# Performance work log

Measured on AMD Instinct MI355X. Metric: run time of the kernel, lower is better.

The kernel has to match this reference:

```python
import jax, jax.numpy as jnp
import numpy as np

BOS = 1  # TOKENS['BOS'] assumed


def gru_scan(x_seq, h0, W_ih, W_hh, b_ih, b_hh):
    """PyTorch-style single-layer GRU over time. x_seq: (T,B,H), h0: (B,H)."""
    def step(h, x):
        gi = x @ W_ih.T + b_ih          # (B,3H)
        gh = h @ W_hh.T + b_hh          # (B,3H)
        i_r, i_z, i_n = jnp.split(gi, 3, axis=-1)
        h_r, h_z, h_n = jnp.split(gh, 3, axis=-1)
        r = jax.nn.sigmoid(i_r + h_r)
        z = jax.nn.sigmoid(i_z + h_z)
        n = jnp.tanh(i_n + r * h_n)
        h_new = (1.0 - z) * n + z * h
        return h_new, h_new
    hT, outs = jax.lax.scan(step, h0, x_seq)
    return outs, hT


def setup_inputs() -> dict:
    key = jax.random.key(0)
    ks = jax.random.split(key, 24)
    H = 256
    V = 50003       # user_size + 3
    TAGV = 966
    T_in, T_tgt, T_tag, B = 50, 40, 20, 32
    s = 0.02
    inp = {
        'input_tensor': jax.random.randint(ks[0], (T_in, B), 0, V),
        'target_tensor': jax.random.randint(ks[1], (T_tgt, B), 0, V),
        'tag_tensor': jax.random.randint(ks[2], (T_tag, B), 0, TAGV),
        'enc_emb': jax.random.normal(ks[3], (V, H), jnp.float32) * s,
        'enc_Wih': jax.random.normal(ks[4], (3 * H, H), jnp.float32) * s,
        'enc_Whh': jax.random.normal(ks[5], (3 * H, H), jnp.float32) * s,
        'enc_bih': jax.random.normal(ks[6], (3 * H,), jnp.float32) * s,
        'enc_bhh': jax.random.normal(ks[7], (3 * H,), jnp.float32) * s,
        'tag_emb': jax.random.normal(ks[8], (TAGV, H), jnp.float32) * s,
        'tag_Wih': jax.random.normal(ks[9], (3 * H, H), jnp.float32) * s,
        'tag_Whh': jax.random.normal(ks[10], (3 * H, H), jnp.float32) * s,
        'tag_bih': jax.random.normal(ks[11], (3 * H,), jnp.float32) * s,
        'tag_bhh': jax.random.normal(ks[12], (3 * H,), jnp.float32) * s,
        'proj_W': jax.random.normal(ks[13], (H, 2 * H), jnp.float32) * s,
        'proj_b': jax.random.normal(ks[14], (H,), jnp.float32) * s,
        'dec_Wih': jax.random.normal(ks[15], (3 * H, H), jnp.float32) * s,
        'dec_Whh': jax.random.normal(ks[16], (3 * H, H), jnp.float32) * s,
        'dec_bih': jax.random.normal(ks[17], (3 * H,), jnp.float32) * s,
        'dec_bhh': jax.random.normal(ks[18], (3 * H,), jnp.float32) * s,
        'out_W': jax.random.normal(ks[19], (V, H), jnp.float32) * s,
        'out_b': jax.random.normal(ks[20], (V,), jnp.float32) * s,
    }
    return inp


def reference(input_tensor, target_tensor, tag_tensor,
              enc_emb, enc_Wih, enc_Whh, enc_bih, enc_bhh,
              tag_emb, tag_Wih, tag_Whh, tag_bih, tag_bhh,
              proj_W, proj_b,
              dec_Wih, dec_Whh, dec_bih, dec_bhh,
              out_W, out_b):
    T_in, B = input_tensor.shape
    T_tgt = target_tensor.shape[0]
    H = enc_emb.shape[1]
    h0 = jnp.zeros((B, H), enc_emb.dtype)

    # encoder over input tokens
    _, enc_h = gru_scan(enc_emb[input_tensor], h0, enc_Wih, enc_Whh, enc_bih, enc_bhh)
    # tag encoder
    _, tag_h = gru_scan(tag_emb[tag_tensor], h0, tag_Wih, tag_Whh, tag_bih, tag_bhh)

    # proj(cat(tag_hidden, encoder_hidden)); dropout = identity (eval)
    merged = jnp.concatenate([tag_h, enc_h], axis=-1) @ proj_W.T + proj_b  # (B,H)

    # teacher forcing: decoder inputs = [BOS, target[:-1]]
    dec_in = jnp.concatenate(
        [jnp.full((1, B), BOS, dtype=target_tensor.dtype), target_tensor[:-1]], axis=0)
    dec_x = jax.nn.relu(enc_emb[dec_in])                 # (T_tgt,B,H), shared embedding
    dec_outs, _ = gru_scan(dec_x, merged, dec_Wih, dec_Whh, dec_bih, dec_bhh)
    logits = dec_outs @ out_W.T + out_b                  # (T_tgt,B,V)

    # criterion = CrossEntropyLoss(mean over batch), summed over timesteps
    logp = jax.nn.log_softmax(logits, axis=-1)
    nll = -jnp.take_along_axis(logp, target_tensor[..., None], axis=-1)[..., 0]  # (T_tgt,B)
    decoder_loss = nll.mean(axis=1).sum()
    avg_loss = decoder_loss / T_tgt
    decoder_outputs = logits[:, None, :, :]              # (T_tgt,1,B,V) like torch.stack of unsqueezed
    return (decoder_loss, avg_loss, decoder_outputs)
```

## Files before the change

kernel.cpp:

```cpp
#include <hip/hip_runtime.h>
#include <hip/hip_bf16.h>
#include <math.h>


#define H 256
#define H3 768
#define NBATCH 32
#define TIN 50
#define TTGT 40
#define TTAG 20
#define VSZ 50003
#define VP 50048
#define NT 782
#define MT 1280
#define NGIET 210
#define NCVT2 504

typedef float f32x4 __attribute__((ext_vector_type(4)));
typedef short short8 __attribute__((ext_vector_type(8)));

__device__ __forceinline__ float dot4(float4 a, float4 b) {
    return a.x * b.x + a.y * b.y + a.z * b.z + a.w * b.w;
}

__device__ __forceinline__ float bf2f(short s) {
    unsigned int u = ((unsigned int)(unsigned short)s) << 16;
    return __builtin_bit_cast(float, u);
}

__device__ __forceinline__ void bar_lgkm() {
    asm volatile("s_waitcnt lgkmcnt(0)" ::: "memory");
    __builtin_amdgcn_s_barrier();
    __builtin_amdgcn_sched_barrier(0);
}

__global__ void k_prep(const float* eWih, const float* tWih, const float* dWih,
                       float* d0, float* d1, float* d2) {
    int which = blockIdx.y;
    const float* s = which == 0 ? eWih : (which == 1 ? tWih : dWih);
    float* d = which == 0 ? d0 : (which == 1 ? d1 : d2);
    int n = blockIdx.x;
    for (int k = threadIdx.x; k < H; k += 256)
        d[(size_t)(k >> 2) * (H3 * 4) + n * 4 + (k & 3)] = s[(size_t)n * H + k];
}

__global__ __launch_bounds__(256) void k_gi_prep(
    const int* in_toks, const int* tag_toks, const float* enc_emb,
    const float* tag_emb, const float* W4e, const float* W4t,
    const float* bih_e, const float* bhh_e, const float* bih_t,
    const float* bhh_t, __hip_bfloat16* gi_e, __hip_bfloat16* gi_t,
    const float* eWhh, const float* tWhh, const float* dWhh,
    __hip_bfloat16* p0, __hip_bfloat16* p1, __hip_bfloat16* p2,
    const float* projW, float* W4_proj) {
    int bx = blockIdx.x, tid = threadIdx.x;
    if (bx >= 498) {
        int n = bx - 498;
        for (int k = tid; k < 2 * H; k += 256)
            W4_proj[(size_t)(k >> 2) * 1024 + n * 4 + (k & 3)] =
                projW[(size_t)n * 2 * H + k];
        return;
    }
    if (bx >= NGIET) {
        int wb = bx - NGIET;
        int m = wb / 96;
        const float* s = m == 0 ? eWhh : (m == 1 ? tWhh : dWhh);
        __hip_bfloat16* d = m == 0 ? p0 : (m == 1 ? p1 : p2);
        int idx = (wb % 96) * 256 + tid;
        int lane = idx & 63;
        int f = (idx >> 6) % 24;
        int w = idx / (24 * 64);
        int ks = f / 3, q = f % 3;
        int row = (q << 8) + (w << 4) + (lane & 15);
        int k = (ks << 5) + ((lane >> 4) << 3);
#pragma unroll
        for (int j = 0; j < 8; ++j)
            d[(size_t)idx * 8 + j] = __float2bfloat16(s[(size_t)row * H + k + j]);
        return;
    }
    __shared__ float x[NBATCH][H];
    int g = bx % 3, tt = bx / 3;
    const int* toks;
    const float* emb;
    const float* W4;
    const float* bihp;
    const float* bhhp;
    __hip_bfloat16* gip;
    int t;
    if (tt < TIN) {
        toks = in_toks; emb = enc_emb; W4 = W4e; bihp = bih_e; bhhp = bhh_e;
        gip = gi_e; t = tt;
    } else {
        toks = tag_toks; emb = tag_emb; W4 = W4t; bihp = bih_t; bhhp = bhh_t;
        gip = gi_t; t = tt - TIN;
    }
    for (int b = 0; b < NBATCH; ++b)
        x[b][tid] = emb[(size_t)toks[t * NBATCH + b] * H + tid];
    __syncthreads();
    int nb_ = tid & 63, mg = tid >> 6;
    float acc[4][8];
#pragma unroll
    for (int j = 0; j < 4; ++j)
#pragma unroll
        for (int mi = 0; mi < 8; ++mi) acc[j][mi] = 0.f;
    for (int k4 = 0; k4 < 64; ++k4) {
        const float4* wrow = (const float4*)(W4 + (size_t)k4 * 3072);
        float4 w0 = wrow[g * 256 + nb_];
        float4 w1 = wrow[g * 256 + nb_ + 64];
        float4 w2 = wrow[g * 256 + nb_ + 128];
        float4 w3 = wrow[g * 256 + nb_ + 192];
#pragma unroll
        for (int mi = 0; mi < 8; ++mi) {
            float4 xv = *(const float4*)&x[mg * 8 + mi][k4 * 4];
            acc[0][mi] += dot4(xv, w0);
            acc[1][mi] += dot4(xv, w1);
            acc[2][mi] += dot4(xv, w2);
            acc[3][mi] += dot4(xv, w3);
        }
    }
#pragma unroll
    for (int j = 0; j < 4; ++j) {
        int n = g * 256 + nb_ + j * 64;
        float bv = bihp[n] + (g < 2 ? bhhp[n] : 0.0f);
        int nn = n & 255;
        int ww = nn >> 4, lrr = nn & 15;
#pragma unroll
        for (int mi = 0; mi < 8; ++mi) {
            int bm = mg * 8 + mi;
            int locb = bm >> 4, lmm = bm & 15;
            int lgg = lmm >> 2, reg = lmm & 3;
            size_t idx = ((size_t)(t * 2 + locb) * 16 + ww) * 1024 +
                         reg * 256 + (lgg * 16 + lrr) * 4 + g;
            gip[idx] = __float2bfloat16(acc[j][mi] + bv);
        }
    }
}

__global__ __launch_bounds__(1024) void k_scan_enc(
    const __hip_bfloat16* gi1, const __hip_bfloat16* W1, const float* bhh1,
    float* hT1, int T1,
    const __hip_bfloat16* gi2, const __hip_bfloat16* W2, const float* bhh2,
    float* hT2, int T2,
    const int* tgt_toks, const float* enc_emb, const float* W4d,
    const float* bih_d, const float* bhh_d, __hip_bfloat16* gi_d,
    const float* outW, __hip_bfloat16* outWb) {
    __shared__ uint4 WL[16 * 6 * 64];
    __shared__ uint4 HBF[2][512];

    int blk = blockIdx.x, tid = threadIdx.x;
    if (blk >= 4) {
        int wb = blk - 4;
        if (wb < TTGT) {
            int t = wb;
            float* x = (float*)WL;
            if (tid < 256) {
                for (int b = 0; b < NBATCH; ++b) {
                    int tok = (t == 0) ? 1 : tgt_toks[(t - 1) * NBATCH + b];
                    x[b * 256 + tid] = fmaxf(enc_emb[(size_t)tok * H + tid], 0.0f);
                }
            }
            __syncthreads();
            if (tid < 768) {
                int g = tid >> 8, tidg = tid & 255;
                int nb_ = tidg & 63, mg = tidg >> 6;
                float acc[4][8];
#pragma unroll
                for (int j = 0; j < 4; ++j)
#pragma unroll
                    for (int mi = 0; mi < 8; ++mi) acc[j][mi] = 0.f;
                for (int k4 = 0; k4 < 64; ++k4) {
                    const float4* wrow = (const float4*)(W4d + (size_t)k4 * 3072);
                    float4 w0 = wrow[g * 256 + nb_];
                    float4 w1 = wrow[g * 256 + nb_ + 64];
                    float4 w2 = wrow[g * 256 + nb_ + 128];
                    float4 w3 = wrow[g * 256 + nb_ + 192];
#pragma unroll
                    for (int mi = 0; mi < 8; ++mi) {
                        float4 xv = *(const float4*)&x[(mg * 8 + mi) * 256 + k4 * 4];
                        acc[0][mi] += dot4(xv, w0);
                        acc[1][mi] += dot4(xv, w1);
                        acc[2][mi] += dot4(xv, w2);
                        acc[3][mi] += dot4(xv, w3);
                    }
                }
#pragma unroll
                for (int j = 0; j < 4; ++j) {
                    int n = g * 256 + nb_ + j * 64;
                    float bv = bih_d[n] + (g < 2 ? bhh_d[n] : 0.0f);
                    int nn = n & 255;
                    int ww = nn >> 4, lrr = nn & 15;
#pragma unroll
                    for (int mi = 0; mi < 8; ++mi) {
                        int bm = mg * 8 + mi;
                        int locb = bm >> 4, lmm = bm & 15;
                        int lgg = lmm >> 2, reg = lmm & 3;
                        size_t idx = ((size_t)(t * 2 + locb) * 16 + ww) * 1024 +
                                     reg * 256 + (lgg * 16 + lrr) * 4 + g;
                        gi_d[idx] = __float2bfloat16(acc[j][mi] + bv);
                    }
                }
            }
            return;
        }
        const size_t total = (size_t)VP * H / 4;
        const size_t stride = (size_t)NCVT2 * 1024;
        for (size_t i = (size_t)(wb - TTGT) * 1024 + tid; i < total; i += stride) {
            size_t i4 = i * 4;
            int row = (int)(i4 >> 8);
            float4 v;
            if (row < VSZ) v = *(const float4*)(outW + i4);
            else v = make_float4(0.f, 0.f, 0.f, 0.f);
            outWb[i4 + 0] = __float2bfloat16(v.x);
            outWb[i4 + 1] = __float2bfloat16(v.y);
            outWb[i4 + 2] = __float2bfloat16(v.z);
            outWb[i4 + 3] = __float2bfloat16(v.w);
        }
        return;
    }

    const __hip_bfloat16 *gip, *Wg;
    const float* bhh;
    float* hTp;
    int T, loc;
    if (blk < 2) {
        gip = gi1; Wg = W1; bhh = bhh1; hTp = hT1; T = T1; loc = blk;
    } else {
        gip = gi2; Wg = W2; bhh = bhh2; hTp = hT2; T = T2; loc = blk - 2;
    }
    int mb = loc * 16;
    int w = tid >> 6, lane = tid & 63, lr = lane & 15, lg = lane >> 4;

    short8 wreg[18];
    const uint4* Wg4 = (const uint4*)Wg;
#pragma unroll
    for (int f = 0; f < 18; ++f) {
        uint4 v = Wg4[(size_t)(w * 24 + f) * 64 + lane];
        wreg[f] = *(short8*)&v;
    }
#pragma unroll
    for (int i = 0; i < 6; ++i)
        WL[(w * 6 + i) * 64 + lane] = Wg4[(size_t)(w * 24 + 18 + i) * 64 + lane];

    float bnv = bhh[512 + w * 16 + lr];

    float hprev[4];
    short* HB16 = (short*)HBF;
#pragma unroll
    for (int reg = 0; reg < 4; ++reg) {
        int row = lg * 4 + reg;
        hprev[reg] = 0.0f;
        int ch = w * 2 + (lr >> 3);
        int slot = ch ^ (row & 7);
        HB16[row * 256 + slot * 8 + (lr & 7)] = 0;
    }
    uint2 gv[4];
    {
        const __hip_bfloat16* gp = gip + ((size_t)loc * 16 + w) * 1024;
#pragma unroll
        for (int reg = 0; reg < 4; ++reg)
            gv[reg] = *(const uint2*)(gp + reg * 256 + lane * 4);
    }
    __syncthreads();

    const short8* HSbase = (const short8*)HBF;
    const short8* WLs = (const short8*)WL;
    for (int t = 0; t < T; ++t) {
        int p = t & 1, p2 = p ^ 1;
        const short8* HS = HSbase + p * 512;
        f32x4 acc[3];
        acc[0] = (f32x4){0.f, 0.f, 0.f, 0.f};
        acc[1] = acc[0];
        acc[2] = (f32x4){bnv, bnv, bnv, bnv};
#pragma unroll
        for (int ks = 0; ks < 6; ++ks) {
            short8 a = HS[lr * 32 + ((ks * 4 + lg) ^ (lr & 7))];
#pragma unroll
            for (int q = 0; q < 3; ++q)
                acc[q] = __builtin_amdgcn_mfma_f32_16x16x32_bf16(
                    a, wreg[ks * 3 + q], acc[q], 0, 0, 0);
        }
#pragma unroll
        for (int ks = 6; ks < 8; ++ks) {
            short8 a = HS[lr * 32 + ((ks * 4 + lg) ^ (lr & 7))];
#pragma unroll
            for (int q = 0; q < 3; ++q) {
                short8 bv = WLs[(w * 6 + (ks - 6) * 3 + q) * 64 + lane];
                acc[q] = __builtin_amdgcn_mfma_f32_16x16x32_bf16(
                    a, bv, acc[q], 0, 0, 0);
            }
        }
#pragma unroll
        for (int reg = 0; reg < 4; ++reg) {
            uint2 u = gv[reg];
            float gr = bf2f((short)(u.x & 0xffff));
            float gz = bf2f((short)(u.x >> 16));
            float gn = bf2f((short)(u.y & 0xffff));
            float er = __expf(-(gr + acc[0][reg]));
            float r = __builtin_amdgcn_rcpf(1.0f + er);
            float ez = __expf(-(gz + acc[1][reg]));
            float z = __builtin_amdgcn_rcpf(1.0f + ez);
            float xx = gn + r * acc[2][reg];
            float e2 = __expf(-2.0f * fabsf(xx));
            float nv = copysignf((1.0f - e2) * __builtin_amdgcn_rcpf(1.0f + e2), xx);
            float hnew = (1.0f - z) * nv + z * hprev[reg];
            hprev[reg] = hnew;
            __hip_bfloat16 qb = __float2bfloat16(hnew);
            int row = lg * 4 + reg;
            int ch = w * 2 + (lr >> 3);
            int slot = ch ^ (row & 7);
            HB16[p2 * 4096 + row * 256 + slot * 8 + (lr & 7)] = *(short*)&qb;
        }
        if (t + 1 < T) {
            const __hip_bfloat16* gp =
                gip + ((size_t)((t + 1) * 2 + loc) * 16 + w) * 1024;
#pragma unroll
            for (int reg = 0; reg < 4; ++reg)
                gv[reg] = *(const uint2*)(gp + reg * 256 + lane * 4);
        }
        bar_lgkm();
    }
    if (hTp) {
#pragma unroll
        for (int reg = 0; reg < 4; ++reg) {
            int row = lg * 4 + reg, col = w * 16 + lr;
            hTp[(size_t)(mb + row) * H + col] = hprev[reg];
        }
    }
}

__global__ __launch_bounds__(1024) void k_scan_dec(
    const __hip_bfloat16* gip, const __hip_bfloat16* Wg, const float* bhh,
    __hip_bfloat16* outp, int T,
    const float* tagh, const float* ench, const float* W4p, const float* pb) {
    __shared__ uint4 WL[16 * 6 * 64];
    __shared__ uint4 HBF[2][512];

    int blk = blockIdx.x, tid = threadIdx.x;
    int loc = blk, mb = loc * 16;
    int w = tid >> 6, lane = tid & 63, lr = lane & 15, lg = lane >> 4;

    float* CC = (float*)WL;
    float* MM = ((float*)WL) + 8192;
#pragma unroll
    for (int i = 0; i < 8; ++i) {
        int idx = i * 1024 + tid;
        int row = idx >> 9, col = idx & 511;
        float v = (col < 256) ? tagh[(size_t)(mb + row) * H + col]
                              : ench[(size_t)(mb + row) * H + (col - 256)];
        CC[idx] = v;
    }
    __syncthreads();
    {
        int col = tid & 255, rg = tid >> 8;
        float a0 = 0.f, a1 = 0.f, a2 = 0.f, a3 = 0.f;
        for (int k4 = 0; k4 < 128; ++k4) {
            float4 wv = ((const float4*)(W4p + (size_t)k4 * 1024))[col];
            float4 c0 = *(const float4*)&CC[(rg * 4 + 0) * 512 + k4 * 4];
            float4 c1 = *(const float4*)&CC[(rg * 4 + 1) * 512 + k4 * 4];
            float4 c2 = *(const float4*)&CC[(rg * 4 + 2) * 512 + k4 * 4];
            float4 c3 = *(const float4*)&CC[(rg * 4 + 3) * 512 + k4 * 4];
            a0 += dot4(c0, wv);
            a1 += dot4(c1, wv);
            a2 += dot4(c2, wv);
            a3 += dot4(c3, wv);
        }
        float bv = pb[col];
        __syncthreads();
        MM[(rg * 4 + 0) * 256 + col] = a0 + bv;
        MM[(rg * 4 + 1) * 256 + col] = a1 + bv;
        MM[(rg * 4 + 2) * 256 + col] = a2 + bv;
        MM[(rg * 4 + 3) * 256 + col] = a3 + bv;
    }
    __syncthreads();

    float hprev[4];
    short* HB16 = (short*)HBF;
#pragma unroll
    for (int reg = 0; reg < 4; ++reg) {
        int row = lg * 4 + reg, col = w * 16 + lr;
        float hv = MM[row * 256 + col];
        hprev[reg] = hv;
        __hip_bfloat16 q = __float2bfloat16(hv);
        int ch = w * 2 + (lr >> 3);
        int slot = ch ^ (row & 7);
        HB16[row * 256 + slot * 8 + (lr & 7)] = *(short*)&q;
    }
    __syncthreads();

    short8 wreg[18];
    const uint4* Wg4 = (const uint4*)Wg;
#pragma unroll
    for (int f = 0; f < 18; ++f) {
        uint4 v = Wg4[(size_t)(w * 24 + f) * 64 + lane];
        wreg[f] = *(short8*)&v;
    }
#pragma unroll
    for (int i = 0; i < 6; ++i)
        WL[(w * 6 + i) * 64 + lane] = Wg4[(size_t)(w * 24 + 18 + i) * 64 + lane];

    float bnv = bhh[512 + w * 16 + lr];

    uint2 gv[4];
    {
        const __hip_bfloat16* gp = gip + ((size_t)loc * 16 + w) * 1024;
#pragma unroll
        for (int reg = 0; reg < 4; ++reg)
            gv[reg] = *(const uint2*)(gp + reg * 256 + lane * 4);
    }
    __syncthreads();

    const short8* HSbase = (const short8*)HBF;
    const short8* WLs = (const short8*)WL;
    for (int t = 0; t < T; ++t) {
        int p = t & 1, p2 = p ^ 1;
        const short8* HS = HSbase + p * 512;
        f32x4 acc[3];
        acc[0] = (f32x4){0.f, 0.f, 0.f, 0.f};
        acc[1] = acc[0];
        acc[2] = (f32x4){bnv, bnv, bnv, bnv};
#pragma unroll
        for (int ks = 0; ks < 6; ++ks) {
            short8 a = HS[lr * 32 + ((ks * 4 + lg) ^ (lr & 7))];
#pragma unroll
            for (int q = 0; q < 3; ++q)
                acc[q] = __builtin_amdgcn_mfma_f32_16x16x32_bf16(
                    a, wreg[ks * 3 + q], acc[q], 0, 0, 0);
        }
#pragma unroll
        for (int ks = 6; ks < 8; ++ks) {
            short8 a = HS[lr * 32 + ((ks * 4 + lg) ^ (lr & 7))];
#pragma unroll
            for (int q = 0; q < 3; ++q) {
                short8 bv = WLs[(w * 6 + (ks - 6) * 3 + q) * 64 + lane];
                acc[q] = __builtin_amdgcn_mfma_f32_16x16x32_bf16(
                    a, bv, acc[q], 0, 0, 0);
            }
        }
#pragma unroll
        for (int reg = 0; reg < 4; ++reg) {
            uint2 u = gv[reg];
            float gr = bf2f((short)(u.x & 0xffff));
            float gz = bf2f((short)(u.x >> 16));
            float gn = bf2f((short)(u.y & 0xffff));
            float er = __expf(-(gr + acc[0][reg]));
            float r = __builtin_amdgcn_rcpf(1.0f + er);
            float ez = __expf(-(gz + acc[1][reg]));
            float z = __builtin_amdgcn_rcpf(1.0f + ez);
            float xx = gn + r * acc[2][reg];
            float e2 = __expf(-2.0f * fabsf(xx));
            float nv = copysignf((1.0f - e2) * __builtin_amdgcn_rcpf(1.0f + e2), xx);
            float hnew = (1.0f - z) * nv + z * hprev[reg];
            hprev[reg] = hnew;
            __hip_bfloat16 qb = __float2bfloat16(hnew);
            int row = lg * 4 + reg;
            int ch = w * 2 + (lr >> 3);
            int slot = ch ^ (row & 7);
            HB16[p2 * 4096 + row * 256 + slot * 8 + (lr & 7)] = *(short*)&qb;
        }
        if (t + 1 < T) {
            const __hip_bfloat16* gp =
                gip + ((size_t)((t + 1) * 2 + loc) * 16 + w) * 1024;
#pragma unroll
            for (int reg = 0; reg < 4; ++reg)
                gv[reg] = *(const uint2*)(gp + reg * 256 + lane * 4);
        }
        if (t >= 1 && tid < 512) {
            int lb = tid >> 5, ch2 = tid & 31;
            short8 hv = HSbase[p * 512 + lb * 32 + (ch2 ^ (lb & 7))];
            *(short8*)(outp + (size_t)((t - 1) * NBATCH + mb + lb) * H + ch2 * 8) = hv;
        }
        bar_lgkm();
    }
    if (tid < 512) {
        int lb = tid >> 5, ch2 = tid & 31;
        short8 hv = HSbase[(T & 1) * 512 + lb * 32 + (ch2 ^ (lb & 7))];
        *(short8*)(outp + (size_t)((T - 1) * NBATCH + mb + lb) * H + ch2 * 8) = hv;
    }
}

__global__ __launch_bounds__(256) void k_logits(const __hip_bfloat16* A,
                                                const __hip_bfloat16* Bw,
                                                const float* bias, float* dout,
                                                float* pmax, float* psum) {
    __shared__ uint4 bsm[2048];
    __shared__ float cst[4][16][68];
    int bid = blockIdx.x;
    int wg = (bid & 7) * 1955 + (bid >> 3);
    int nblk = wg / 20, mblk = wg % 20;
    int m0 = mblk * 64, n0 = nblk * 64;
    int tid = threadIdx.x;
    int wave = tid >> 6, lane = tid & 63, lr = lane & 15, lg = lane >> 4;
    const uint4* Bg = (const uint4*)(Bw + (size_t)n0 * H);
#pragma unroll
    for (int i = 0; i < 8; ++i) {
        int c = tid + i * 256;
        int r = c >> 5, g = c & 31;
        bsm[(r << 5) | (g ^ (r & 7))] = Bg[c];
    }
    short8 areg[8];
    const uint4* Ar = (const uint4*)(A + (size_t)(m0 + wave * 16 + lr) * H);
#pragma unroll
    for (int ks = 0; ks < 8; ++ks) {
        uint4 v = Ar[ks * 4 + lg];
        areg[ks] = *(short8*)&v;
    }
    float biasv[4];
    bool valid[4];
#pragma unroll
    for (int ns = 0; ns < 4; ++ns) {
        int n = n0 + ns * 16 + lr;
        valid[ns] = (n < VSZ);
        biasv[ns] = valid[ns] ? bias[n] : 0.f;
    }
    __syncthreads();
    f32x4 acc[4];
#pragma unroll
    for (int ns = 0; ns < 4; ++ns) acc[ns] = (f32x4){0.f, 0.f, 0.f, 0.f};
    const short8* L = (const short8*)bsm;
#pragma unroll
    for (int ks = 0; ks < 8; ++ks) {
        int ga = ks * 4 + lg;
#pragma unroll
        for (int ns = 0; ns < 4; ++ns) {
            int rb = ns * 16 + lr;
            acc[ns] = __builtin_amdgcn_mfma_f32_16x16x32_bf16(
                areg[ks], L[(rb << 5) | (ga ^ (rb & 7))], acc[ns], 0, 0, 0);
        }
    }
    float* cw = &cst[wave][0][0];
#pragma unroll
    for (int reg = 0; reg < 4; ++reg) {
        int m = m0 + wave * 16 + lg * 4 + reg;
        float v[4];
        float rm = -INFINITY;
#pragma unroll
        for (int ns = 0; ns < 4; ++ns) {
            v[ns] = acc[ns][reg] + biasv[ns];
            if (valid[ns]) rm = fmaxf(rm, v[ns]);
            cw[(lg * 4 + reg) * 68 + ns * 16 + lr] = v[ns];
        }
        for (int off = 1; off < 16; off <<= 1) rm = fmaxf(rm, __shfl_xor(rm, off));
        float se = 0.f;
#pragma unroll
        for (int ns = 0; ns < 4; ++ns)
            if (valid[ns]) se += __expf(v[ns] - rm);
        for (int off = 1; off < 16; off <<= 1) se += __shfl_xor(se, off);
        if (lr == 0) {
            pmax[(size_t)m * NT + nblk] = rm;
            psum[(size_t)m * NT + nblk] = se;
        }
    }
    float* dbase = dout + 2 + (size_t)(m0 + wave * 16) * VSZ + n0;
    int c0 = lr * 4;
    bool full = (n0 + c0 + 3 < VSZ);
#pragma unroll
    for (int it = 0; it < 4; ++it) {
        int row = it * 4 + lg;
        f32x4 v4 = *(const f32x4*)&cst[wave][row][c0];
        float* p = dbase + (size_t)row * VSZ + c0;
        if (full) {
            __builtin_memcpy(p, &v4, 16);
        } else {
#pragma unroll
            for (int j = 0; j < 4; ++j)
                if (n0 + c0 + j < VSZ) p[j] = v4[j];
        }
    }
}

__global__ void k_lse(const float* pmax, const float* psum, float* lse) {
    int m = blockIdx.x, tid = threadIdx.x;
    __shared__ float sm[4];
    float lm = -INFINITY;
    for (int i = tid; i < NT; i += 256) lm = fmaxf(lm, pmax[(size_t)m * NT + i]);
    for (int off = 1; off < 64; off <<= 1) lm = fmaxf(lm, __shfl_xor(lm, off));
    if ((tid & 63) == 0) sm[tid >> 6] = lm;
    __syncthreads();
    float M = fmaxf(fmaxf(sm[0], sm[1]), fmaxf(sm[2], sm[3]));
    __syncthreads();
    float s = 0.f;
    for (int i = tid; i < NT; i += 256)
        s += psum[(size_t)m * NT + i] * __expf(pmax[(size_t)m * NT + i] - M);
    for (int off = 1; off < 64; off <<= 1) s += __shfl_xor(s, off);
    if ((tid & 63) == 0) sm[tid >> 6] = s;
    __syncthreads();
    if (tid == 0) lse[m] = M + logf(sm[0] + sm[1] + sm[2] + sm[3]);
}

__global__ void k_loss(const float* lse, const int* tgt, float* dout) {
    int tid = threadIdx.x;
    __shared__ float sm[4];
    float s = 0.f;
    for (int m = tid; m < MT; m += 256) {
        int tg = tgt[m];
        s += lse[m] - dout[2 + (size_t)m * VSZ + tg];
    }
    for (int off = 1; off < 64; off <<= 1) s += __shfl_xor(s, off);
    if ((tid & 63) == 0) sm[tid >> 6] = s;
    __syncthreads();
    if (tid == 0) {
        float total = sm[0] + sm[1] + sm[2] + sm[3];
        dout[0] = total / 32.0f;
        dout[1] = total / 1280.0f;
    }
}

extern "C" void kernel_launch(void* const* d_in, const int* in_sizes, int n_in,
                              void* d_out, int out_size, void* d_ws,
                              size_t ws_size, hipStream_t stream) {
    const int* input_tensor = (const int*)d_in[0];
    const int* target_tensor = (const int*)d_in[1];
    const int* tag_tensor = (const int*)d_in[2];
    const float* enc_emb = (const float*)d_in[3];
    const float* enc_Wih = (const float*)d_in[4];
    const float* enc_Whh = (const float*)d_in[5];
    const float* enc_bih = (const float*)d_in[6];
    const float* enc_bhh = (const float*)d_in[7];
    const float* tag_emb = (const float*)d_in[8];
    const float* tag_Wih = (const float*)d_in[9];
    const float* tag_Whh = (const float*)d_in[10];
    const float* tag_bih = (const float*)d_in[11];
    const float* tag_bhh = (const float*)d_in[12];
    const float* proj_W = (const float*)d_in[13];
    const float* proj_b = (const float*)d_in[14];
    const float* dec_Wih = (const float*)d_in[15];
    const float* dec_Whh = (const float*)d_in[16];
    const float* dec_bih = (const float*)d_in[17];
    const float* dec_bhh = (const float*)d_in[18];
    const float* out_W = (const float*)d_in[19];
    const float* out_b = (const float*)d_in[20];

    char* wsb = (char*)d_ws;
    size_t o = 0;
    auto alloc = [&](size_t bytes) {
        size_t r = o;
        o += (bytes + 511) & ~(size_t)511;
        return r;
    };
    float* W4_enc_ih = (float*)(wsb + alloc(H3 * H * 4));
    float* W4_tag_ih = (float*)(wsb + alloc(H3 * H * 4));
    float* W4_dec_ih = (float*)(wsb + alloc(H3 * H * 4));
    float* W4_proj   = (float*)(wsb + alloc(H * 2 * H * 4));
    __hip_bfloat16* gi_enc = (__hip_bfloat16*)(wsb + alloc((size_t)TIN * 65536));
    __hip_bfloat16* gi_tag = (__hip_bfloat16*)(wsb + alloc((size_t)TTAG * 65536));
    __hip_bfloat16* gi_dec = (__hip_bfloat16*)(wsb + alloc((size_t)TTGT * 65536));
    float* enc_h  = (float*)(wsb + alloc(NBATCH * H * 4));
    float* tag_h  = (float*)(wsb + alloc(NBATCH * H * 4));
    float* lse    = (float*)(wsb + alloc(MT * 4));
    __hip_bfloat16* Wp_enc = (__hip_bfloat16*)(wsb + alloc(H3 * H * 2));
    __hip_bfloat16* Wp_tag = (__hip_bfloat16*)(wsb + alloc(H3 * H * 2));
    __hip_bfloat16* Wp_dec = (__hip_bfloat16*)(wsb + alloc(H3 * H * 2));
    __hip_bfloat16* outWb  = (__hip_bfloat16*)(wsb + alloc((size_t)VP * H * 2));
    __hip_bfloat16* decA   = (__hip_bfloat16*)(wsb + alloc((size_t)MT * H * 2));
    float* pmax = (float*)(wsb + alloc((size_t)MT * NT * 4));
    float* psum = (float*)(wsb + alloc((size_t)MT * NT * 4));

    float* dout = (float*)d_out;

    k_prep<<<dim3(H3, 3), 256, 0, stream>>>(enc_Wih, tag_Wih, dec_Wih,
                                            W4_enc_ih, W4_tag_ih, W4_dec_ih);

    k_gi_prep<<<754, 256, 0, stream>>>(
        input_tensor, tag_tensor, enc_emb, tag_emb, W4_enc_ih, W4_tag_ih,
        enc_bih, enc_bhh, tag_bih, tag_bhh, gi_enc, gi_tag,
        enc_Whh, tag_Whh, dec_Whh, Wp_enc, Wp_tag, Wp_dec, proj_W, W4_proj);

    k_scan_enc<<<4 + TTGT + NCVT2, 1024, 0, stream>>>(
        gi_enc, Wp_enc, enc_bhh, enc_h, TIN,
        gi_tag, Wp_tag, tag_bhh, tag_h, TTAG,
        target_tensor, enc_emb, W4_dec_ih, dec_bih, dec_bhh, gi_dec,
        out_W, outWb);

    k_scan_dec<<<2, 1024, 0, stream>>>(gi_dec, Wp_dec, dec_bhh, decA, TTGT,
                                       tag_h, enc_h, W4_proj, proj_b);

    k_logits<<<NT * 20, 256, 0, stream>>>(decA, outWb, out_b, dout, pmax, psum);

    k_lse<<<MT, 256, 0, stream>>>(pmax, psum, lse);

    k_loss<<<1, 256, 0, stream>>>(lse, target_tensor, dout);
}
```

Measured before the change: 424.0 us.

## Fuse decoder scan with logits GEMM using progress flags to overlap

Merges the two-block decoder GRU scan and the vocabulary logits GEMM into one kernel. Blocks 0-1 run the scan and publish a per-8-timestep progress counter through replicated atomic flags, and the remaining blocks spin-wait until their 256-row chunk of decoder outputs is ready before computing logits. The aim is to overlap the output projection with the serial recurrence and remove a kernel launch boundary. The risks are deadlock if the scan blocks are not scheduled before the waiting blocks fill the GPU, plus polling overhead and the larger 1024-thread logits tiles with 112KB of shared memory lowering occupancy.

New measurement: 576.0 us. +35.8%, slower.

```diff
diff --git a/kernel.cpp b/kernel.cpp
--- a/kernel.cpp
+++ b/kernel.cpp
@@ -35,8 +35,11 @@
 }
 
 __global__ void k_prep(const float* eWih, const float* tWih, const float* dWih,
-                       float* d0, float* d1, float* d2) {
+                       float* d0, float* d1, float* d2, int* progrep) {
     int which = blockIdx.y;
+    if (which == 0 && blockIdx.x == 0) {
+        for (int i = threadIdx.x; i < 1024; i += 256) progrep[i] = 0;
+    }
     const float* s = which == 0 ? eWih : (which == 1 ? tWih : dWih);
     float* d = which == 0 ? d0 : (which == 1 ? d1 : d2);
     int n = blockIdx.x;
@@ -327,16 +330,120 @@
     }
 }
 
-__global__ __launch_bounds__(1024) void k_scan_dec(
+__global__ __launch_bounds__(1024) void k_declog(
     const __hip_bfloat16* gip, const __hip_bfloat16* Wg, const float* bhh,
-    __hip_bfloat16* outp, int T,
-    const float* tagh, const float* ench, const float* W4p, const float* pb) {
-    __shared__ uint4 WL[16 * 6 * 64];
-    __shared__ uint4 HBF[2][512];
-
-    int blk = blockIdx.x, tid = threadIdx.x;
-    int loc = blk, mb = loc * 16;
-    int w = tid >> 6, lane = tid & 63, lr = lane & 15, lg = lane >> 4;
+    __hip_bfloat16* decA, int* progrep,
+    const float* tagh, const float* ench, const float* W4p, const float* pb,
+    const __hip_bfloat16* Bw, const float* bias, float* dout,
+    float* pmax, float* psum) {
+    __shared__ __align__(16) char smem[114688];
+    int tid = threadIdx.x;
+    int wave = tid >> 6, lane = tid & 63, lr = lane & 15, lg = lane >> 4;
+
+    if (blockIdx.x >= 2) {
+        uint4* bsm = (uint4*)smem;
+        float* cst = (float*)(smem + 32768);
+        int lb = blockIdx.x - 2;
+        int quad = lb / NT, nblk = lb % NT;
+        int wq = wave >> 2, wsub = wave & 3;
+        int m0 = quad * 256 + wq * 64;
+        int n0 = nblk * 64;
+        const uint4* Bg = (const uint4*)(Bw + (size_t)n0 * H);
+#pragma unroll
+        for (int i = 0; i < 2; ++i) {
+            int c = tid + i * 1024;
+            int r = c >> 5, g = c & 31;
+            bsm[(r << 5) | (g ^ (r & 7))] = Bg[c];
+        }
+        float biasv[4];
+        bool valid[4];
+#pragma unroll
+        for (int ns = 0; ns < 4; ++ns) {
+            int n = n0 + ns * 16 + lr;
+            valid[ns] = (n < VSZ);
+            biasv[ns] = valid[ns] ? bias[n] : 0.f;
+        }
+        if (tid == 0) {
+            int need = quad * 8 + 8;
+            int line = (blockIdx.x & 63) * 16;
+            while (true) {
+                int p0 = __hip_atomic_load(&progrep[line + 0], __ATOMIC_ACQUIRE,
+                                           __HIP_MEMORY_SCOPE_AGENT);
+                int p1 = __hip_atomic_load(&progrep[line + 1], __ATOMIC_ACQUIRE,
+                                           __HIP_MEMORY_SCOPE_AGENT);
+                if (p0 >= need && p1 >= need) break;
+                for (int s = 0; s < 8; ++s) __builtin_amdgcn_s_sleep(64);
+            }
+        }
+        __syncthreads();
+        short8 areg[8];
+        const uint4* Ar = (const uint4*)(decA + (size_t)(m0 + wsub * 16 + lr) * H);
+#pragma unroll
+        for (int ks = 0; ks < 8; ++ks) {
+            uint4 v = Ar[ks * 4 + lg];
+            areg[ks] = *(short8*)&v;
+        }
+        f32x4 acc[4];
+#pragma unroll
+        for (int ns = 0; ns < 4; ++ns) acc[ns] = (f32x4){0.f, 0.f, 0.f, 0.f};
+        const short8* L = (const short8*)bsm;
+#pragma unroll
+        for (int ks = 0; ks < 8; ++ks) {
+            int ga = ks * 4 + lg;
+#pragma unroll
+            for (int ns = 0; ns < 4; ++ns) {
+                int rb = ns * 16 + lr;
+                acc[ns] = __builtin_amdgcn_mfma_f32_16x16x32_bf16(
+                    areg[ks], L[(rb << 5) | (ga ^ (rb & 7))], acc[ns], 0, 0, 0);
+            }
+        }
+        float* cw = cst + wave * (16 * 68);
+#pragma unroll
+        for (int reg = 0; reg < 4; ++reg) {
+            int m = m0 + wsub * 16 + lg * 4 + reg;
+            float v[4];
+            float rm = -INFINITY;
+#pragma unroll
+            for (int ns = 0; ns < 4; ++ns) {
+                v[ns] = acc[ns][reg] + biasv[ns];
+                if (valid[ns]) rm = fmaxf(rm, v[ns]);
+                cw[(lg * 4 + reg) * 68 + ns * 16 + lr] = v[ns];
+            }
+            for (int off = 1; off < 16; off <<= 1) rm = fmaxf(rm, __shfl_xor(rm, off));
+            float se = 0.f;
+#pragma unroll
+            for (int ns = 0; ns < 4; ++ns)
+                if (valid[ns]) se += __expf(v[ns] - rm);
+            for (int off = 1; off < 16; off <<= 1) se += __shfl_xor(se, off);
+            if (lr == 0) {
+                pmax[(size_t)m * NT + nblk] = rm;
+                psum[(size_t)m * NT + nblk] = se;
+            }
+        }
+        float* dbase = dout + 2 + (size_t)(m0 + wsub * 16) * VSZ + n0;
+        int c0 = lr * 4;
+        bool full = (n0 + c0 + 3 < VSZ);
+#pragma unroll
+        for (int it = 0; it < 4; ++it) {
+            int row = it * 4 + lg;
+            f32x4 v4 = *(const f32x4*)&cw[row * 68 + c0];
+            float* pp = dbase + (size_t)row * VSZ + c0;
+            if (full) {
+                __builtin_memcpy(pp, &v4, 16);
+            } else {
+#pragma unroll
+                for (int j = 0; j < 4; ++j)
+                    if (n0 + c0 + j < VSZ) pp[j] = v4[j];
+            }
+        }
+        return;
+    }
+
+    uint4* WL = (uint4*)smem;
+    uint4* HBF = (uint4*)(smem + 98304);
+    int loc = blockIdx.x, mb = loc * 16;
+    int w = wave;
+    const int T = TTGT;
 
     float* CC = (float*)WL;
     float* MM = ((float*)WL) + 8192;
@@ -464,106 +571,32 @@
                 gv[reg] = *(const uint2*)(gp + reg * 256 + lane * 4);
         }
         if (t >= 1 && tid < 512) {
-            int lb = tid >> 5, ch2 = tid & 31;
-            short8 hv = HSbase[p * 512 + lb * 32 + (ch2 ^ (lb & 7))];
-            *(short8*)(outp + (size_t)((t - 1) * NBATCH + mb + lb) * H + ch2 * 8) = hv;
-        }
+            int lb2 = tid >> 5, ch2 = tid & 31;
+            short8 hv = HSbase[p * 512 + lb2 * 32 + (ch2 ^ (lb2 & 7))];
+            *(short8*)(decA + (size_t)((t - 1) * NBATCH + mb + lb2) * H + ch2 * 8) = hv;
+        }
+        bool pub = (t >= 8) && ((t & 7) == 0);
+        if (pub) asm volatile("s_waitcnt vmcnt(0)" ::: "memory");
         bar_lgkm();
+        if (pub && tid == 0) {
+            __threadfence();
+            for (int i = 0; i < 64; ++i)
+                __hip_atomic_store(&progrep[i * 16 + loc], t, __ATOMIC_RELEASE,
+                                   __HIP_MEMORY_SCOPE_AGENT);
+        }
     }
     if (tid < 512) {
-        int lb = tid >> 5, ch2 = tid & 31;
-        short8 hv = HSbase[(T & 1) * 512 + lb * 32 + (ch2 ^ (lb & 7))];
-        *(short8*)(outp + (size_t)((T - 1) * NBATCH + mb + lb) * H + ch2 * 8) = hv;
-    }
-}
-
-__global__ __launch_bounds__(256) void k_logits(const __hip_bfloat16* A,
-                                                const __hip_bfloat16* Bw,
-                                                const float* bias, float* dout,
-                                                float* pmax, float* psum) {
-    __shared__ uint4 bsm[2048];
-    __shared__ float cst[4][16][68];
-    int bid = blockIdx.x;
-    int wg = (bid & 7) * 1955 + (bid >> 3);
-    int nblk = wg / 20, mblk = wg % 20;
-    int m0 = mblk * 64, n0 = nblk * 64;
-    int tid = threadIdx.x;
-    int wave = tid >> 6, lane = tid & 63, lr = lane & 15, lg = lane >> 4;
-    const uint4* Bg = (const uint4*)(Bw + (size_t)n0 * H);
-#pragma unroll
-    for (int i = 0; i < 8; ++i) {
-        int c = tid + i * 256;
-        int r = c >> 5, g = c & 31;
-        bsm[(r << 5) | (g ^ (r & 7))] = Bg[c];
-    }
-    short8 areg[8];
-    const uint4* Ar = (const uint4*)(A + (size_t)(m0 + wave * 16 + lr) * H);
-#pragma unroll
-    for (int ks = 0; ks < 8; ++ks) {
-        uint4 v = Ar[ks * 4 + lg];
-        areg[ks] = *(short8*)&v;
-    }
-    float biasv[4];
-    bool valid[4];
-#pragma unroll
-    for (int ns = 0; ns < 4; ++ns) {
-        int n = n0 + ns * 16 + lr;
-        valid[ns] = (n < VSZ);
-        biasv[ns] = valid[ns] ? bias[n] : 0.f;
-    }
-    __syncthreads();
-    f32x4 acc[4];
-#pragma unroll
-    for (int ns = 0; ns < 4; ++ns) acc[ns] = (f32x4){0.f, 0.f, 0.f, 0.f};
-    const short8* L = (const short8*)bsm;
-#pragma unroll
-    for (int ks = 0; ks < 8; ++ks) {
-        int ga = ks * 4 + lg;
-#pragma unroll
-        for (int ns = 0; ns < 4; ++ns) {
-            int rb = ns * 16 + lr;
-            acc[ns] = __builtin_amdgcn_mfma_f32_16x16x32_bf16(
-                areg[ks], L[(rb << 5) | (ga ^ (rb & 7))], acc[ns], 0, 0, 0);
-        }
-    }
-    float* cw = &cst[wave][0][0];
-#pragma unroll
-    for (int reg = 0; reg < 4; ++reg) {
-        int m = m0 + wave * 16 + lg * 4 + reg;
-        float v[4];
-        float rm = -INFINITY;
-#pragma unroll
-        for (int ns = 0; ns < 4; ++ns) {
-            v[ns] = acc[ns][reg] + biasv[ns];
-            if (valid[ns]) rm = fmaxf(rm, v[ns]);
-            cw[(lg * 4 + reg) * 68 + ns * 16 + lr] = v[ns];
-        }
-        for (int off = 1; off < 16; off <<= 1) rm = fmaxf(rm, __shfl_xor(rm, off));
-        float se = 0.f;
-#pragma unroll
-        for (int ns = 0; ns < 4; ++ns)
-            if (valid[ns]) se += __expf(v[ns] - rm);
-        for (int off = 1; off < 16; off <<= 1) se += __shfl_xor(se, off);
-        if (lr == 0) {
-            pmax[(size_t)m * NT + nblk] = rm;
-            psum[(size_t)m * NT + nblk] = se;
-        }
-    }
-    float* dbase = dout + 2 + (size_t)(m0 + wave * 16) * VSZ + n0;
-    int c0 = lr * 4;
-    bool full = (n0 + c0 + 3 < VSZ);
-#pragma unroll
-    for (int it = 0; it < 4; ++it) {
-        int row = it * 4 + lg;
-        f32x4 v4 = *(const f32x4*)&cst[wave][row][c0];
-        float* p = dbase + (size_t)row * VSZ + c0;
-        if (full) {
-            __builtin_memcpy(p, &v4, 16);
-        } else {
-#pragma unroll
-            for (int j = 0; j < 4; ++j)
-                if (n0 + c0 + j < VSZ) p[j] = v4[j];
-        }
+        int lb2 = tid >> 5, ch2 = tid & 31;
+        short8 hv = HSbase[(T & 1) * 512 + lb2 * 32 + (ch2 ^ (lb2 & 7))];
+        *(short8*)(decA + (size_t)((T - 1) * NBATCH + mb + lb2) * H + ch2 * 8) = hv;
+    }
+    asm volatile("s_waitcnt vmcnt(0)" ::: "memory");
+    __syncthreads();
+    if (tid == 0) {
+        __threadfence();
+        for (int i = 0; i < 64; ++i)
+            __hip_atomic_store(&progrep[i * 16 + loc], TTGT, __ATOMIC_RELEASE,
+                               __HIP_MEMORY_SCOPE_AGENT);
     }
 }
 
@@ -646,6 +679,7 @@
     float* enc_h  = (float*)(wsb + alloc(NBATCH * H * 4));
     float* tag_h  = (float*)(wsb + alloc(NBATCH * H * 4));
     float* lse    = (float*)(wsb + alloc(MT * 4));
+    int*   progrep = (int*)(wsb + alloc(1024 * 4));
     __hip_bfloat16* Wp_enc = (__hip_bfloat16*)(wsb + alloc(H3 * H * 2));
     __hip_bfloat16* Wp_tag = (__hip_bfloat16*)(wsb + alloc(H3 * H * 2));
     __hip_bfloat16* Wp_dec = (__hip_bfloat16*)(wsb + alloc(H3 * H * 2));
@@ -657,7 +691,8 @@
     float* dout = (float*)d_out;
 
     k_prep<<<dim3(H3, 3), 256, 0, stream>>>(enc_Wih, tag_Wih, dec_Wih,
-                                            W4_enc_ih, W4_tag_ih, W4_dec_ih);
+                                            W4_enc_ih, W4_tag_ih, W4_dec_ih,
+                                            progrep);
 
     k_gi_prep<<<754, 256, 0, stream>>>(
         input_tensor, tag_tensor, enc_emb, tag_emb, W4_enc_ih, W4_tag_ih,
@@ -670,10 +705,10 @@
         target_tensor, enc_emb, W4_dec_ih, dec_bih, dec_bhh, gi_dec,
         out_W, outWb);
 
-    k_scan_dec<<<2, 1024, 0, stream>>>(gi_dec, Wp_dec, dec_bhh, decA, TTGT,
-                                       tag_h, enc_h, W4_proj, proj_b);
-
-    k_logits<<<NT * 20, 256, 0, stream>>>(decA, outWb, out_b, dout, pmax, psum);
+    k_declog<<<2 + 5 * NT, 1024, 0, stream>>>(
+        gi_dec, Wp_dec, dec_bhh, decA, progrep,
+        tag_h, enc_h, W4_proj, proj_b,
+        outWb, out_b, dout, pmax, psum);
 
     k_lse<<<MT, 256, 0, stream>>>(pmax, psum, lse);
 
```
